# Performance work log

Measured on AMD Instinct MI355X. Metric: run time of the kernel, lower is better.

## Reference

```python
import jax, jax.numpy as jnp
import numpy as np

B, D_IN, N = 128, 1024, 1024  # batch, input feature dim, output_dim


def setup_inputs() -> dict:
    key = jax.random.key(0)
    k1, k2, k3 = jax.random.split(key, 3)
    des = jax.random.normal(k1, (B, D_IN), dtype=jnp.float32)
    body = jax.random.normal(k2, (B, D_IN), dtype=jnp.float32)
    # keras 'uniform' initializer: RandomUniform(-0.05, 0.05)
    kernel = jax.random.uniform(k3, (D_IN, N), dtype=jnp.float32,
                                minval=-0.05, maxval=0.05)
    return {"des": des, "body": body, "kernel": kernel}


def _circulant_matvec(v, u):
    # Faithful to circulant(v) @ u from the original layer:
    # circ[b, k, j] = v[b, (k - j) mod n]  (column j of the circulant matrix is
    # v rolled down by j), then batch_dot over j -> circular convolution.
    n = v.shape[1]
    i = jnp.arange(n)
    idx = (i[:, None] - i[None, :]) % n        # (n, n) gather indices
    circ = v[:, idx]                           # (B, n, n)
    return jnp.einsum('bkj,bj->bk', circ, u)   # (B, n)


def reference(des, body, kernel):
    d = des @ kernel    # (B, N)
    b = body @ kernel   # (B, N)
    mv1 = _circulant_matvec(b, d)  # batch_dot(circulant(body'), des')
    mv2 = _circulant_matvec(d, b)  # batch_dot(circulant(des'), body')
    # Note: original computes K.dot(sum_vector, kernel) into sum_vector_1 but
    # returns sum_vector, so that dead op is omitted.
    return mv1 + mv2
```

## Files before the change

### kernel.cpp

```cpp
#include <hip/hip_runtime.h>


using bf16x8 = __attribute__((ext_vector_type(8))) short;
using f32x4  = __attribute__((ext_vector_type(4))) float;

static __device__ __forceinline__ unsigned cvt_pk_bf16(float lo, float hi) {
    unsigned r;
    asm("v_cvt_pk_bf16_f32 %0, %1, %2" : "=v"(r) : "v"(lo), "v"(hi));
    return r;
}

__global__ __launch_bounds__(512) void gemm_kernel(
    const float* __restrict__ des, const float* __restrict__ body,
    const float* __restrict__ kmat, float* __restrict__ Ppart)
{
    __shared__ float smem[9216];
    short* Bl = (short*)smem;
    float* Rbuf = smem;

    const int tid = threadIdx.x;
    const int bid = blockIdx.x;
    const int kh = bid & 1;
    const int ct = (bid >> 1) & 31;
    const int rt = bid >> 6;
    const int R0 = rt * 32, C0 = ct * 32;
    const int kb = kh * 512;
    const float* Arow = (R0 < 128) ? (des + (size_t)R0 * 1024)
                                   : (body + (size_t)(R0 - 128) * 1024);

    const int lane = tid & 63;
    const int w = tid >> 6;
    const int lr = lane & 15;
    const int lk = lane >> 4;

    f32x4 acc[2][2];
    #pragma unroll
    for (int q = 0; q < 2; ++q)
        #pragma unroll
        for (int g = 0; g < 2; ++g) acc[q][g] = (f32x4){0.f, 0.f, 0.f, 0.f};

    #pragma unroll
    for (int i = 0; i < 4; ++i) {
        int t4 = tid + i * 512;
        int ke2 = t4 >> 3, c4 = t4 & 7;
        int k = ke2 * 2;
        const float* src = kmat + (size_t)(kb + k) * 1024 + C0 + c4 * 4;
        float4 Fa = *(const float4*)src;
        float4 Fb = *(const float4*)(src + 1024);
        const float fa[4] = {Fa.x, Fa.y, Fa.z, Fa.w};
        const float fb[4] = {Fb.x, Fb.y, Fb.z, Fb.w};
        int kg = (k >> 3) & 3, kc = k >> 5, sw = (k >> 3) & 7;
        #pragma unroll
        for (int u = 0; u < 4; ++u) {
            int c = c4 * 4 + u;
            int unit = (((c >> 4) * 16 + kc) << 6) + (kg << 4) + ((c & 15) ^ sw);
            *(unsigned*)&Bl[unit * 8 + (k & 7)] = cvt_pk_bf16(fa[u], fb[u]);
        }
    }
    __syncthreads();

    #pragma unroll
    for (int s = 0; s < 2; ++s) {
        const int kc = w * 2 + s;
        const int kglob = kb + kc * 32 + lk * 8;

        bf16x8 afr[2];
        #pragma unroll
        for (int q = 0; q < 2; ++q) {
            const float* ap = Arow + (size_t)(q * 16 + lr) * 1024 + kglob;
            float4 F0 = *(const float4*)ap;
            float4 F1 = *(const float4*)(ap + 4);
            uint4 ua;
            ua.x = cvt_pk_bf16(F0.x, F0.y);
            ua.y = cvt_pk_bf16(F0.z, F0.w);
            ua.z = cvt_pk_bf16(F1.x, F1.y);
            ua.w = cvt_pk_bf16(F1.z, F1.w);
            afr[q] = *(bf16x8*)&ua;
        }
        const int slot = lr ^ ((kc * 4 + lk) & 7);
        #pragma unroll
        for (int g = 0; g < 2; ++g) {
            int unit = ((g * 16 + kc) << 6) + (lk << 4) + slot;
            bf16x8 bfr = *(const bf16x8*)&Bl[unit * 8];
            acc[0][g] = __builtin_amdgcn_mfma_f32_16x16x32_bf16(bfr, afr[0], acc[0][g], 0, 0, 0);
            acc[1][g] = __builtin_amdgcn_mfma_f32_16x16x32_bf16(bfr, afr[1], acc[1][g], 0, 0, 0);
        }
    }
    __syncthreads();

    #pragma unroll
    for (int q = 0; q < 2; ++q)
        #pragma unroll
        for (int g = 0; g < 2; ++g) {
            int r = q * 16 + lr;
            int c = g * 16 + (lk << 2);
            *(f32x4*)&Rbuf[w * 1152 + r * 36 + c] = acc[q][g];
        }
    __syncthreads();
    {
        int o = tid * 2;
        int r = o >> 5, c = o & 31;
        float2 s = make_float2(0.f, 0.f);
        #pragma unroll
        for (int u = 0; u < 8; ++u) {
            float2 v = *(const float2*)&Rbuf[u * 1152 + r * 36 + c];
            s.x += v.x; s.y += v.y;
        }
        *(float2*)(Ppart + (size_t)kh * 262144 + (size_t)(R0 + r) * 1024 + C0 + c) = s;
    }
}

__global__ __launch_bounds__(512) void conv_kernel(
    const float* __restrict__ Ppart, float* __restrict__ out)
{
    __shared__ float dl[1024];
    __shared__ float bl[1024];
    __shared__ float red[4608];

    const int tid = threadIdx.x;
    const int bid = blockIdx.x;
    const int r = bid >> 1;
    const int h = bid & 1;

    {
        int isB = tid >> 8, i4 = tid & 255;
        const float4* s0 = (const float4*)(Ppart + (size_t)(isB ? 128 + r : r) * 1024);
        const float4* s1 = (const float4*)(Ppart + 262144 + (size_t)(isB ? 128 + r : r) * 1024);
        float4 a = s0[i4], b = s1[i4];
        float4 v = make_float4(a.x + b.x, a.y + b.y, a.z + b.z, a.w + b.w);
        if (isB) ((float4*)bl)[i4] = v;
        else     ((float4*)dl)[i4 ^ ((i4 >> 3) & 7)] = v;
    }
    __syncthreads();

    const int jo = tid >> 6;
    const int t  = tid & 63;
    const int k0 = (h * 512 + t * 8 - jo * 128) & 1023;

#define RD(fidx) (((const float4*)dl)[(((fidx) >> 2) ^ ((((fidx) >> 2) >> 3) & 7))])

    float acc[8] = {0.f, 0.f, 0.f, 0.f, 0.f, 0.f, 0.f, 0.f};
    float4 A  = RD(k0);
    float4 Bv = RD((k0 + 4) & 1023);

    const float* bq = bl + jo * 128;
    #pragma unroll 4
    for (int jc = 0; jc < 128; jc += 4) {
        float4 bv = *(const float4*)&bq[jc];
        float4 Nv = RD((k0 - jc - 4) & 1023);
        acc[0] += bv.x * A.x;  acc[1] += bv.x * A.y;  acc[2] += bv.x * A.z;  acc[3] += bv.x * A.w;
        acc[4] += bv.x * Bv.x; acc[5] += bv.x * Bv.y; acc[6] += bv.x * Bv.z; acc[7] += bv.x * Bv.w;
        acc[0] += bv.y * Nv.w; acc[1] += bv.y * A.x;  acc[2] += bv.y * A.y;  acc[3] += bv.y * A.z;
        acc[4] += bv.y * A.w;  acc[5] += bv.y * Bv.x; acc[6] += bv.y * Bv.y; acc[7] += bv.y * Bv.z;
        acc[0] += bv.z * Nv.z; acc[1] += bv.z * Nv.w; acc[2] += bv.z * A.x;  acc[3] += bv.z * A.y;
        acc[4] += bv.z * A.z;  acc[5] += bv.z * A.w;  acc[6] += bv.z * Bv.x; acc[7] += bv.z * Bv.y;
        acc[0] += bv.w * Nv.y; acc[1] += bv.w * Nv.z; acc[2] += bv.w * Nv.w; acc[3] += bv.w * A.x;
        acc[4] += bv.w * A.y;  acc[5] += bv.w * A.z;  acc[6] += bv.w * A.w;  acc[7] += bv.w * Bv.x;
        Bv = A; A = Nv;
    }
#undef RD

    {
        float* rd = red + jo * 576 + t * 9;
        #pragma unroll
        for (int q = 0; q < 8; ++q) rd[q] = acc[q];
    }
    __syncthreads();
    {
        int tt = tid >> 3, qq = tid & 7;
        float s = 0.f;
        #pragma unroll
        for (int u = 0; u < 8; ++u) s += red[u * 576 + tt * 9 + qq];
        out[(size_t)r * 1024 + h * 512 + tid] = 2.f * s;
    }
}

extern "C" void kernel_launch(void* const* d_in, const int* in_sizes, int n_in,
                              void* d_out, int out_size, void* d_ws, size_t ws_size,
                              hipStream_t stream) {
    const float* des  = (const float*)d_in[0];
    const float* body = (const float*)d_in[1];
    const float* kmat = (const float*)d_in[2];
    float* Ppart = (float*)d_ws;

    gemm_kernel<<<512, 512, 0, stream>>>(des, body, kmat, Ppart);
    conv_kernel<<<256, 512, 0, stream>>>(Ppart, (float*)d_out);
}
```

Baseline: 17.74 us.

## Retile circular convolution to 16 outputs per thread with 4 blocks per row

The conv kernel now gives each thread a register tile of 16 outputs over a 64-wide j chunk, instead of 8 outputs over a 128-wide chunk. This raises FMA reuse per LDS load. Each row is split into four 256-output blocks of 256 threads, and the dl swizzle and the reduction layout change to match. The larger register window raises register pressure. The block count doubles while total threads stay the same, and the reduction now sums 16 partials.

Measured after the change: 18.01 us. No clear change (+1.6%).

```diff
diff --git a/kernel.cpp b/kernel.cpp
--- a/kernel.cpp
+++ b/kernel.cpp
@@ -110,68 +110,78 @@
     }
 }
 
-__global__ __launch_bounds__(512) void conv_kernel(
+__global__ __launch_bounds__(256) void conv_kernel(
     const float* __restrict__ Ppart, float* __restrict__ out)
 {
     __shared__ float dl[1024];
     __shared__ float bl[1024];
-    __shared__ float red[4608];
+    __shared__ float red[4352];
 
     const int tid = threadIdx.x;
     const int bid = blockIdx.x;
-    const int r = bid >> 1;
-    const int h = bid & 1;
+    const int r = bid >> 2;
+    const int kq = bid & 3;
 
     {
-        int isB = tid >> 8, i4 = tid & 255;
-        const float4* s0 = (const float4*)(Ppart + (size_t)(isB ? 128 + r : r) * 1024);
-        const float4* s1 = (const float4*)(Ppart + 262144 + (size_t)(isB ? 128 + r : r) * 1024);
-        float4 a = s0[i4], b = s1[i4];
-        float4 v = make_float4(a.x + b.x, a.y + b.y, a.z + b.z, a.w + b.w);
-        if (isB) ((float4*)bl)[i4] = v;
-        else     ((float4*)dl)[i4 ^ ((i4 >> 3) & 7)] = v;
+        const float* Pd0 = Ppart + (size_t)r * 1024;
+        const float* Pd1 = Pd0 + 262144;
+        const float* Pb0 = Ppart + (size_t)(128 + r) * 1024;
+        const float* Pb1 = Pb0 + 262144;
+        float4 a = ((const float4*)Pd0)[tid], b = ((const float4*)Pd1)[tid];
+        ((float4*)dl)[tid ^ ((tid >> 2) & 7)] =
+            make_float4(a.x + b.x, a.y + b.y, a.z + b.z, a.w + b.w);
+        float4 e = ((const float4*)Pb0)[tid], f = ((const float4*)Pb1)[tid];
+        ((float4*)bl)[tid] =
+            make_float4(e.x + f.x, e.y + f.y, e.z + f.z, e.w + f.w);
     }
     __syncthreads();
 
-    const int jo = tid >> 6;
-    const int t  = tid & 63;
-    const int k0 = (h * 512 + t * 8 - jo * 128) & 1023;
+    const int jg = tid >> 4;
+    const int t  = tid & 15;
+    const int k0 = (kq * 256 + t * 16 - jg * 64) & 1023;
 
-#define RD(fidx) (((const float4*)dl)[(((fidx) >> 2) ^ ((((fidx) >> 2) >> 3) & 7))])
+#define RD(fidx) (((const float4*)dl)[(((fidx) >> 2) ^ ((((fidx) >> 2) >> 2) & 7))])
 
-    float acc[8] = {0.f, 0.f, 0.f, 0.f, 0.f, 0.f, 0.f, 0.f};
-    float4 A  = RD(k0);
-    float4 Bv = RD((k0 + 4) & 1023);
+    float c[20];
+    { float4 v = RD((k0 - 4) & 1023); c[0]=v.x; c[1]=v.y; c[2]=v.z; c[3]=v.w; }
+    { float4 v = RD(k0);              c[4]=v.x; c[5]=v.y; c[6]=v.z; c[7]=v.w; }
+    { float4 v = RD((k0+4) & 1023);   c[8]=v.x; c[9]=v.y; c[10]=v.z; c[11]=v.w; }
+    { float4 v = RD((k0+8) & 1023);   c[12]=v.x; c[13]=v.y; c[14]=v.z; c[15]=v.w; }
+    { float4 v = RD((k0+12) & 1023);  c[16]=v.x; c[17]=v.y; c[18]=v.z; c[19]=v.w; }
 
-    const float* bq = bl + jo * 128;
-    #pragma unroll 4
-    for (int jc = 0; jc < 128; jc += 4) {
-        float4 bv = *(const float4*)&bq[jc];
-        float4 Nv = RD((k0 - jc - 4) & 1023);
-        acc[0] += bv.x * A.x;  acc[1] += bv.x * A.y;  acc[2] += bv.x * A.z;  acc[3] += bv.x * A.w;
-        acc[4] += bv.x * Bv.x; acc[5] += bv.x * Bv.y; acc[6] += bv.x * Bv.z; acc[7] += bv.x * Bv.w;
-        acc[0] += bv.y * Nv.w; acc[1] += bv.y * A.x;  acc[2] += bv.y * A.y;  acc[3] += bv.y * A.z;
-        acc[4] += bv.y * A.w;  acc[5] += bv.y * Bv.x; acc[6] += bv.y * Bv.y; acc[7] += bv.y * Bv.z;
-        acc[0] += bv.z * Nv.z; acc[1] += bv.z * Nv.w; acc[2] += bv.z * A.x;  acc[3] += bv.z * A.y;
-        acc[4] += bv.z * A.z;  acc[5] += bv.z * A.w;  acc[6] += bv.z * Bv.x; acc[7] += bv.z * Bv.y;
-        acc[0] += bv.w * Nv.y; acc[1] += bv.w * Nv.z; acc[2] += bv.w * Nv.w; acc[3] += bv.w * A.x;
-        acc[4] += bv.w * A.y;  acc[5] += bv.w * A.z;  acc[6] += bv.w * A.w;  acc[7] += bv.w * Bv.x;
-        Bv = A; A = Nv;
+    float acc[16];
+    #pragma unroll
+    for (int q = 0; q < 16; ++q) acc[q] = 0.f;
+
+    const float* bq = bl + jg * 64;
+    #pragma unroll
+    for (int jc = 0; jc < 64; jc += 4) {
+        float4 bv4 = *(const float4*)&bq[jc];
+        float4 Nv = RD((k0 - jc - 8) & 1023);
+        const float bs[4] = {bv4.x, bv4.y, bv4.z, bv4.w};
+        #pragma unroll
+        for (int s = 0; s < 4; ++s)
+            #pragma unroll
+            for (int q = 0; q < 16; ++q)
+                acc[q] += bs[s] * c[q + 4 - s];
+        #pragma unroll
+        for (int i = 19; i >= 4; --i) c[i] = c[i - 4];
+        c[0] = Nv.x; c[1] = Nv.y; c[2] = Nv.z; c[3] = Nv.w;
     }
 #undef RD
 
     {
-        float* rd = red + jo * 576 + t * 9;
+        float* rd = red + tid * 17;
         #pragma unroll
-        for (int q = 0; q < 8; ++q) rd[q] = acc[q];
+        for (int q = 0; q < 16; ++q) rd[q] = acc[q];
     }
     __syncthreads();
     {
-        int tt = tid >> 3, qq = tid & 7;
+        int base = ((tid >> 4)) * 17 + (tid & 15);
         float s = 0.f;
         #pragma unroll
-        for (int u = 0; u < 8; ++u) s += red[u * 576 + tt * 9 + qq];
-        out[(size_t)r * 1024 + h * 512 + tid] = 2.f * s;
+        for (int u = 0; u < 16; ++u) s += red[u * 272 + base];
+        out[(size_t)r * 1024 + kq * 256 + tid] = 2.f * s;
     }
 }
 
@@ -184,5 +194,5 @@
     float* Ppart = (float*)d_ws;
 
     gemm_kernel<<<512, 512, 0, stream>>>(des, body, kmat, Ppart);
-    conv_kernel<<<256, 512, 0, stream>>>(Ppart, (float*)d_out);
+    conv_kernel<<<512, 256, 0, stream>>>(Ppart, (float*)d_out);
 }
```
